# Kernel optimization log

Measured on AMD Instinct MI355X. Metric: run time of the kernel, lower is better.

The kernel has to match this reference:

```python
import jax, jax.numpy as jnp
import numpy as np

HID = 4096      # hidden_size
H = 32          # num_attention_heads
K = 8           # num_key_value_heads
D = HID // H    # head_dim = 128
G = H // K      # q heads per kv group = 4
INTER = 14336   # intermediate_size
T = 2048        # tokens (prefill)
EPS = 1e-5
THETA = 1000000.0


def setup_inputs() -> dict:
    key = jax.random.key(0)
    ks = jax.random.split(key, 9)
    s = 0.02
    return {
        "hidden_states": jax.random.normal(ks[0], (T, HID), jnp.float32),
        "position_ids": jnp.arange(T, dtype=jnp.int64),
        "wqkv": jax.random.normal(ks[1], ((H + 2 * K) * D, HID), jnp.float32) * s,
        "wo": jax.random.normal(ks[2], (HID, HID), jnp.float32) * s,
        "w1": jax.random.normal(ks[3], (INTER, HID), jnp.float32) * s,  # gate
        "w3": jax.random.normal(ks[4], (INTER, HID), jnp.float32) * s,  # up
        "w2": jax.random.normal(ks[5], (HID, INTER), jnp.float32) * s,  # down
        "attn_norm_w": jnp.ones((HID,), jnp.float32),
        "ffn_norm_w": jnp.ones((HID,), jnp.float32),
    }


def _rmsnorm(x, w):
    var = jnp.mean(jnp.square(x), axis=-1, keepdims=True)
    return x * jax.lax.rsqrt(var + EPS) * w


def _rope(x, cos, sin):
    # non-interleaved (half-split) rotation; x: [T, h, D], cos/sin: [T, 1, D//2]
    x1, x2 = x[..., : D // 2], x[..., D // 2 :]
    return jnp.concatenate([x1 * cos - x2 * sin, x2 * cos + x1 * sin], axis=-1)


def _attention(x, position_ids, wqkv, wo):
    t = x.shape[0]
    qkv = x @ wqkv.T  # [T, (H+2K)*D]
    q = qkv[:, : H * D].reshape(t, H, D)
    k = qkv[:, H * D : (H + K) * D].reshape(t, K, D)
    v = qkv[:, (H + K) * D :].reshape(t, K, D)

    inv_freq = 1.0 / (THETA ** (jnp.arange(0, D, 2, dtype=jnp.float32) / D))
    freqs = position_ids.astype(jnp.float32)[:, None] * inv_freq  # [T, D//2]
    cos = jnp.cos(freqs)[:, None, :]
    sin = jnp.sin(freqs)[:, None, :]
    q = _rope(q, cos, sin)
    k = _rope(k, cos, sin)

    # grouped-query attention: [T, K, G, D] queries vs [T, K, D] keys
    qg = q.reshape(t, K, G, D)
    scale = 1.0 / jnp.sqrt(jnp.float32(D))
    scores = jnp.einsum("tkgd,skd->kgts", qg, k) * scale  # [K, G, T, T]
    causal = jnp.tril(jnp.ones((t, t), dtype=bool))
    scores = jnp.where(causal, scores, jnp.finfo(scores.dtype).min)
    probs = jax.nn.softmax(scores, axis=-1)
    out = jnp.einsum("kgts,skd->tkgd", probs, v).reshape(t, H * D)
    return out @ wo.T


def _mlp(x, w1, w3, w2):
    return (jax.nn.silu(x @ w1.T) * (x @ w3.T)) @ w2.T


def reference(hidden_states, position_ids, wqkv, wo, w1, w3, w2, attn_norm_w, ffn_norm_w):
    h = hidden_states + _attention(_rmsnorm(hidden_states, attn_norm_w), position_ids, wqkv, wo)
    return h + _mlp(_rmsnorm(h, ffn_norm_w), w1, w3, w2)
```

## Files before the change

kernel.cpp:

```cpp
#include <hip/hip_runtime.h>
#include <stdint.h>

#define T_SEQ 2048
#define HIDN  4096
#define NH    32
#define NKV   8
#define DH    128
#define INTER 14336
#define QKV_N 6144
#define EPSR  1e-5f
#define SCALE 0.08838834764831845f
#define KVB   64

typedef __bf16 bf16x8 __attribute__((ext_vector_type(8)));
typedef float  f32x4  __attribute__((ext_vector_type(4)));

__device__ __forceinline__ f32x4 mfma16(bf16x8 a, bf16x8 b, f32x4 c) {
  return __builtin_amdgcn_mfma_f32_16x16x32_bf16(a, b, c, 0, 0, 0);
}

__device__ __forceinline__ void glds16(const void* g, void* l) {
  __builtin_amdgcn_global_load_lds(
      (__attribute__((address_space(1))) void*)g,
      (__attribute__((address_space(3))) void*)l,
      16, 0, 0);
}

__global__ __launch_bounds__(256) void cvt_bf16_kernel(
    const float* __restrict__ src, __bf16* __restrict__ dst, long n) {
  long stride = (long)gridDim.x * 256 * 8;
  for (long i = ((long)blockIdx.x * 256 + threadIdx.x) * 8; i < n; i += stride) {
    float4 a = *(const float4*)(src + i);
    float4 b = *(const float4*)(src + i + 4);
    bf16x8 o;
    o[0]=(__bf16)a.x; o[1]=(__bf16)a.y; o[2]=(__bf16)a.z; o[3]=(__bf16)a.w;
    o[4]=(__bf16)b.x; o[5]=(__bf16)b.y; o[6]=(__bf16)b.z; o[7]=(__bf16)b.w;
    *(bf16x8*)(dst + i) = o;
  }
}

__global__ __launch_bounds__(256) void rmsnorm_kernel(
    const float* __restrict__ x, const float* __restrict__ w,
    __bf16* __restrict__ y) {
  const int row = blockIdx.x, tid = threadIdx.x;
  const float* xr = x + (size_t)row * HIDN + tid * 16;
  float4 v0 = ((const float4*)xr)[0];
  float4 v1 = ((const float4*)xr)[1];
  float4 v2 = ((const float4*)xr)[2];
  float4 v3 = ((const float4*)xr)[3];
  float ss = v0.x*v0.x + v0.y*v0.y + v0.z*v0.z + v0.w*v0.w
           + v1.x*v1.x + v1.y*v1.y + v1.z*v1.z + v1.w*v1.w
           + v2.x*v2.x + v2.y*v2.y + v2.z*v2.z + v2.w*v2.w
           + v3.x*v3.x + v3.y*v3.y + v3.z*v3.z + v3.w*v3.w;
  #pragma unroll
  for (int off = 32; off >= 1; off >>= 1) ss += __shfl_xor(ss, off, 64);
  __shared__ float red[4];
  if ((tid & 63) == 0) red[tid >> 6] = ss;
  __syncthreads();
  float rn = rsqrtf((red[0] + red[1] + red[2] + red[3]) * (1.0f / HIDN) + EPSR);
  const float* wr = w + tid * 16;
  float4 w0 = ((const float4*)wr)[0];
  float4 w1v = ((const float4*)wr)[1];
  float4 w2v = ((const float4*)wr)[2];
  float4 w3v = ((const float4*)wr)[3];
  bf16x8 o0, o1;
  o0[0]=(__bf16)(v0.x*rn*w0.x);  o0[1]=(__bf16)(v0.y*rn*w0.y);
  o0[2]=(__bf16)(v0.z*rn*w0.z);  o0[3]=(__bf16)(v0.w*rn*w0.w);
  o0[4]=(__bf16)(v1.x*rn*w1v.x); o0[5]=(__bf16)(v1.y*rn*w1v.y);
  o0[6]=(__bf16)(v1.z*rn*w1v.z); o0[7]=(__bf16)(v1.w*rn*w1v.w);
  o1[0]=(__bf16)(v2.x*rn*w2v.x); o1[1]=(__bf16)(v2.y*rn*w2v.y);
  o1[2]=(__bf16)(v2.z*rn*w2v.z); o1[3]=(__bf16)(v2.w*rn*w2v.w);
  o1[4]=(__bf16)(v3.x*rn*w3v.x); o1[5]=(__bf16)(v3.y*rn*w3v.y);
  o1[6]=(__bf16)(v3.z*rn*w3v.z); o1[7]=(__bf16)(v3.w*rn*w3v.w);
  __bf16* yo = y + (size_t)row * HIDN + tid * 16;
  *(bf16x8*)(yo)     = o0;
  *(bf16x8*)(yo + 8) = o1;
}

template<int EPI>
__global__ __launch_bounds__(512, 2) void gemm256_kernel(
    const __bf16* __restrict__ A, const __bf16* __restrict__ B,
    void* __restrict__ Cout, int M, int N, int Kfull, int KZ) {
  extern __shared__ __align__(16) char smem[];
  const int tid = threadIdx.x;
  const int lane = tid & 63;
  const int wv = tid >> 6;
  const int wm = wv >> 2;
  const int wn = wv & 3;
  const int lr = lane & 15, q = lane >> 4;

  const int gx = gridDim.x, gy = gridDim.y;
  const int nwg = gx * gy;
  const int orig = blockIdx.y * gx + blockIdx.x;
  const int cpx = nwg >> 3;
  const int swz = (orig & 7) * cpx + (orig >> 3);
  const int by = swz % gy, bx = swz / gy;
  const int m0 = by * 256, n0 = bx * 256;
  const int kbase = blockIdx.z * KZ;
  const int NT = KZ >> 5;

  const char* aS[2]; const char* bS[2]; int Lds[2];
  #pragma unroll
  for (int j = 0; j < 2; j++) {
    int L = j * 512 + tid;
    int row = L >> 2;
    int s = (L & 3) ^ ((row >> 1) & 3);
    aS[j] = (const char*)(A + (size_t)(m0 + row) * Kfull + kbase + s * 8);
    bS[j] = (const char*)(B + (size_t)(n0 + row) * Kfull + kbase + s * 8);
    Lds[j] = L * 16;
  }

  const int sA = q ^ ((lr >> 1) & 3);
  int aoff[8], boff[4];
  #pragma unroll
  for (int mt = 0; mt < 8; mt++) aoff[mt] = (wm * 128 + mt * 16 + lr) * 64 + sA * 16;
  #pragma unroll
  for (int nt = 0; nt < 4; nt++) boff[nt] = 16384 + (wn * 64 + nt * 16 + lr) * 64 + sA * 16;

#define STAGE_T(tile, sb) do {                                   \
    char* _b = smem + (sb) * 32768;                              \
    size_t _ko = (size_t)(tile) * 64;                            \
    glds16(aS[0] + _ko, _b + Lds[0]);                            \
    glds16(aS[1] + _ko, _b + Lds[1]);                            \
    glds16(bS[0] + _ko, _b + 16384 + Lds[0]);                    \
    glds16(bS[1] + _ko, _b + 16384 + Lds[1]);                    \
  } while (0)

#define GBODY(VMC, DOST) do {                                    \
    if (DOST) { STAGE_T(t + 3, sbufi); sbufi = (sbufi == 4) ? 0 : sbufi + 1; } \
    asm volatile("s_waitcnt vmcnt(" #VMC ")" ::: "memory");      \
    __builtin_amdgcn_s_barrier();                                \
    asm volatile("" ::: "memory");                               \
    __builtin_amdgcn_sched_barrier(0);                           \
    { const char* _bA = smem + bufi * 32768;                     \
      bf16x8 bf[4], af[8];                                       \
      _Pragma("unroll") for (int nt = 0; nt < 4; nt++)           \
        bf[nt] = *(const bf16x8*)(_bA + boff[nt]);               \
      _Pragma("unroll") for (int mt = 0; mt < 8; mt++)           \
        af[mt] = *(const bf16x8*)(_bA + aoff[mt]);               \
      __builtin_amdgcn_s_setprio(1);                             \
      _Pragma("unroll") for (int mt = 0; mt < 8; mt++)           \
        _Pragma("unroll") for (int nt = 0; nt < 4; nt++)         \
          acc[mt][nt] = mfma16(af[mt], bf[nt], acc[mt][nt]);     \
      __builtin_amdgcn_s_setprio(0); }                           \
    bufi = (bufi == 4) ? 0 : bufi + 1;                           \
  } while (0)

  f32x4 acc[8][4] = {};
  STAGE_T(0, 0); STAGE_T(1, 1); STAGE_T(2, 2);
  int bufi = 0, sbufi = 3;
  for (int t = 0; t < NT - 3; ++t) GBODY(12, true);
  { int t = 0; (void)t;
    GBODY(8, false); GBODY(4, false); GBODY(0, false); }
#undef STAGE_T
#undef GBODY

  #pragma unroll
  for (int mt = 0; mt < 8; mt++) {
    #pragma unroll
    for (int r = 0; r < 4; r++) {
      int rr = m0 + wm * 128 + mt * 16 + q * 4 + r;
      #pragma unroll
      for (int nt = 0; nt < 4; nt++) {
        int cc = n0 + wn * 64 + nt * 16 + lr;
        size_t ix = (size_t)rr * N + cc;
        float val = acc[mt][nt][r];
        if (EPI == 0) ((float*)Cout)[(size_t)blockIdx.z * M * N + ix] = val;
        else          ((__bf16*)Cout)[ix] = (__bf16)val;
      }
    }
  }
}

__global__ __launch_bounds__(256) void add3_kernel(
    const float* __restrict__ p, const float* __restrict__ r,
    float* __restrict__ o, long n) {
  long stride = (long)gridDim.x * 1024;
  for (long i = ((long)blockIdx.x * 256 + threadIdx.x) * 4; i < n; i += stride) {
    float4 a = *(const float4*)(p + i);
    float4 b = *(const float4*)(p + n + i);
    float4 c = *(const float4*)(r + i);
    float4 o4;
    o4.x = a.x + b.x + c.x; o4.y = a.y + b.y + c.y;
    o4.z = a.z + b.z + c.z; o4.w = a.w + b.w + c.w;
    *(float4*)(o + i) = o4;
  }
}

__global__ __launch_bounds__(256) void rope_kernel(
    const __bf16* __restrict__ qkv, __bf16* __restrict__ q_r,
    __bf16* __restrict__ k_r) {
  const int t = blockIdx.x, tid = threadIdx.x;
  __shared__ float cs[64], sn[64];
  if (tid < 64) {
    float inv = exp2f(-(float)tid * (19.931568569324174f / 64.0f));
    float f = (float)t * inv;
    cs[tid] = cosf(f);
    sn[tid] = sinf(f);
  }
  __syncthreads();
  const __bf16* row = qkv + (size_t)t * QKV_N;
  for (int it = tid; it < 40 * 64; it += 256) {
    int hh = it >> 6, i = it & 63;
    float x1 = (float)row[hh * 128 + i];
    float x2 = (float)row[hh * 128 + 64 + i];
    float c = cs[i], s = sn[i];
    float o1 = x1 * c - x2 * s;
    float o2 = x2 * c + x1 * s;
    if (hh < NH) {
      __bf16* qo = q_r + (size_t)t * HIDN + hh * 128;
      qo[i] = (__bf16)o1;
      qo[64 + i] = (__bf16)o2;
    } else {
      __bf16* ko = k_r + (size_t)t * (NKV * DH) + (hh - NH) * 128;
      ko[i] = (__bf16)o1;
      ko[64 + i] = (__bf16)o2;
    }
  }
}

__global__ __launch_bounds__(256) void vtrans_kernel(
    const __bf16* __restrict__ qkv, __bf16* __restrict__ v_t) {
  __shared__ __bf16 tile[64][136];
  const int tid = threadIdx.x;
  const int t0 = blockIdx.x * 64, kh = blockIdx.y;
  #pragma unroll
  for (int i = 0; i < 4; i++) {
    int u = i * 256 + tid;
    int row = u >> 4, c = (u & 15) * 8;
    *(bf16x8*)&tile[row][c] =
        *(const bf16x8*)(qkv + (size_t)(t0 + row) * QKV_N + (NH + NKV) * DH + kh * DH + c);
  }
  __syncthreads();
  const int d = tid & 127, th = (tid >> 7) * 32;
  #pragma unroll
  for (int j = 0; j < 4; j++) {
    int t = th + j * 8;
    bf16x8 o;
    #pragma unroll
    for (int e = 0; e < 8; e++) o[e] = tile[t + e][d];
    *(bf16x8*)(v_t + ((size_t)kh * DH + d) * T_SEQ + t0 + t) = o;
  }
}

__global__ __launch_bounds__(256) void attn_kernel(
    const __bf16* __restrict__ q_r, const __bf16* __restrict__ k_r,
    const __bf16* __restrict__ v_t, __bf16* __restrict__ attn_o) {
  __shared__ __align__(16) __bf16 Ks[KVB * 128];
  __shared__ __align__(16) __bf16 Vs[128 * KVB];
  __shared__ __align__(16) __bf16 Pl[4 * 16 * KVB];

  const int tid = threadIdx.x;
  const int lane = tid & 63, wv = tid >> 6;
  const int lr = lane & 15, g = lane >> 4;
  const int qt = gridDim.x - 1 - blockIdx.x;
  const int h = blockIdx.y;
  const int kh = h >> 2;
  const int q0b = qt * 64;
  const int q0w = q0b + wv * 16;

  bf16x8 qf[4];
  {
    const __bf16* qp = q_r + (size_t)(q0w + lr) * HIDN + h * DH + g * 8;
    #pragma unroll
    for (int kk = 0; kk < 4; kk++) qf[kk] = *(const bf16x8*)(qp + kk * 32);
  }

  f32x4 o[8] = {};
  float mrun[4] = {-1e30f, -1e30f, -1e30f, -1e30f};
  float lrun[4] = {0.f, 0.f, 0.f, 0.f};
  char* PlW = (char*)Pl + wv * 2048;

  for (int kv0 = 0; kv0 < q0b + KVB; kv0 += KVB) {
    __syncthreads();
    #pragma unroll
    for (int i = 0; i < 4; i++) {
      int u = i * 256 + tid;
      int row = u >> 4;
      int cb = ((u & 15) * 16) ^ ((row & 7) << 4);
      glds16((const char*)(k_r + (size_t)(kv0 + row) * (NKV * DH) + kh * DH) + cb,
             (char*)Ks + u * 16);
    }
    #pragma unroll
    for (int i = 0; i < 4; i++) {
      int u = i * 256 + tid;
      int row = u >> 3;
      int cb = ((u & 7) * 16) ^ ((row & 7) << 4);
      glds16((const char*)(v_t + ((size_t)kh * DH + row) * T_SEQ + kv0) + cb,
             (char*)Vs + u * 16);
    }
    __syncthreads();

    if (q0w + 15 >= kv0) {
      f32x4 s[4] = {};
      #pragma unroll
      for (int kk = 0; kk < 4; kk++) {
        #pragma unroll
        for (int jt = 0; jt < 4; jt++) {
          int krow = jt * 16 + lr;
          int cb = (kk * 64 + g * 16) ^ ((krow & 7) << 4);
          bf16x8 kf = *(const bf16x8*)((char*)Ks + krow * 256 + cb);
          s[jt] = mfma16(qf[kk], kf, s[jt]);
        }
      }
      const bool need_mask = (kv0 + KVB - 1) > q0w;
      #pragma unroll
      for (int r = 0; r < 4; r++) {
        int qpos = q0w + g * 4 + r;
        int prow = g * 4 + r;
        float p[4];
        #pragma unroll
        for (int jt = 0; jt < 4; jt++) {
          float v = s[jt][r] * SCALE;
          if (need_mask && (kv0 + jt * 16 + lr > qpos)) v = -1e30f;
          p[jt] = v;
        }
        float mx = fmaxf(fmaxf(p[0], p[1]), fmaxf(p[2], p[3]));
        #pragma unroll
        for (int off = 1; off < 16; off <<= 1) mx = fmaxf(mx, __shfl_xor(mx, off, 64));
        float mn = fmaxf(mrun[r], mx);
        float corr = __expf(mrun[r] - mn);
        mrun[r] = mn;
        float ps = 0.f;
        #pragma unroll
        for (int jt = 0; jt < 4; jt++) {
          p[jt] = __expf(p[jt] - mn);
          ps += p[jt];
          int cbyte = ((jt * 16 + lr) * 2) ^ ((prow & 7) << 4);
          *(__bf16*)(PlW + prow * 128 + cbyte) = (__bf16)p[jt];
        }
        #pragma unroll
        for (int off = 1; off < 16; off <<= 1) ps += __shfl_xor(ps, off, 64);
        lrun[r] = lrun[r] * corr + ps;
        #pragma unroll
        for (int nt = 0; nt < 8; nt++) o[nt][r] *= corr;
      }
      bf16x8 pa[2];
      #pragma unroll
      for (int ks = 0; ks < 2; ks++)
        pa[ks] = *(const bf16x8*)(PlW + lr * 128 + ((g * 16 + ks * 64) ^ ((lr & 7) << 4)));
      #pragma unroll
      for (int nt = 0; nt < 8; nt++) {
        #pragma unroll
        for (int ks = 0; ks < 2; ks++) {
          int vrow = nt * 16 + lr;
          int cb = (ks * 64 + g * 16) ^ ((vrow & 7) << 4);
          bf16x8 vf = *(const bf16x8*)((char*)Vs + vrow * 128 + cb);
          o[nt] = mfma16(pa[ks], vf, o[nt]);
        }
      }
    }
  }

  #pragma unroll
  for (int nt = 0; nt < 8; nt++) {
    #pragma unroll
    for (int r = 0; r < 4; r++) {
      int qrow = q0w + g * 4 + r;
      int d = nt * 16 + lr;
      attn_o[(size_t)qrow * HIDN + h * DH + d] = (__bf16)(o[nt][r] / lrun[r]);
    }
  }
}

__global__ __launch_bounds__(256) void silu_mul_kernel(
    const __bf16* __restrict__ u, const __bf16* __restrict__ v,
    __bf16* __restrict__ g, long n) {
  long stride = (long)gridDim.x * 256 * 8;
  for (long i = ((long)blockIdx.x * 256 + threadIdx.x) * 8; i < n; i += stride) {
    bf16x8 uu = *(const bf16x8*)(u + i);
    bf16x8 vv = *(const bf16x8*)(v + i);
    bf16x8 gg;
    #pragma unroll
    for (int j = 0; j < 8; j++) {
      float x = (float)uu[j];
      float y = (float)vv[j];
      float sl = x / (1.0f + __expf(-x));
      gg[j] = (__bf16)(sl * y);
    }
    *(bf16x8*)(g + i) = gg;
  }
}

extern "C" void kernel_launch(void* const* d_in, const int* in_sizes, int n_in,
                              void* d_out, int out_size, void* d_ws, size_t ws_size,
                              hipStream_t stream) {
  const float* hidden = (const float*)d_in[0];
  const float* wqkv = (const float*)d_in[2];
  const float* wo   = (const float*)d_in[3];
  const float* w1   = (const float*)d_in[4];
  const float* w3   = (const float*)d_in[5];
  const float* w2   = (const float*)d_in[6];
  const float* anw  = (const float*)d_in[7];
  const float* fnw  = (const float*)d_in[8];

  char* ws = (char*)d_ws;
  const size_t SZ_XN   = (size_t)T_SEQ * HIDN * 2;
  const size_t SZ_QKV  = (size_t)T_SEQ * QKV_N * 2;
  const size_t SZ_KR   = (size_t)T_SEQ * NKV * DH * 2;
  const size_t SZ_H    = (size_t)T_SEQ * HIDN * 4;
  const size_t SZ_UV   = (size_t)T_SEQ * INTER * 2;

  const size_t W_QKV = (size_t)QKV_N * HIDN * 2;
  const size_t W_O   = (size_t)HIDN * HIDN * 2;
  const size_t W_I   = (size_t)INTER * HIDN * 2;
  const size_t W_TOTAL = W_QKV + W_O + 3 * W_I;

  char* act = ws + W_TOTAL;

  __bf16* xn1    = (__bf16*)(act);
  __bf16* qkv    = (__bf16*)(act + SZ_XN);
  __bf16* q_r    = (__bf16*)(act + SZ_XN + SZ_QKV);
  __bf16* ubuf   = (__bf16*)(act);
  __bf16* k_r    = (__bf16*)(act + SZ_UV);
  __bf16* attn_o = (__bf16*)(act + SZ_UV + SZ_KR);
  float*  hbuf   = (float*) (act + SZ_UV + SZ_KR + SZ_XN);
  __bf16* v_t    = (__bf16*)(act + SZ_UV + SZ_KR + SZ_XN);
  __bf16* xn2    = (__bf16*)(act + SZ_UV + SZ_KR + SZ_XN + SZ_H);
  __bf16* vbuf   = (__bf16*)(act + SZ_UV + SZ_KR + SZ_XN + SZ_H + SZ_XN);
  __bf16* gbuf   = ubuf;
  float*  pbuf   = (float*)(act + SZ_UV + SZ_KR + SZ_XN + SZ_H);

  __bf16* wqkv_b = (__bf16*)(ws);
  __bf16* wo_b   = (__bf16*)(ws + W_QKV);
  __bf16* w1_b   = (__bf16*)(ws + W_QKV + W_O);
  __bf16* w3_b   = (__bf16*)(ws + W_QKV + W_O + W_I);
  __bf16* w2_b   = (__bf16*)(ws + W_QKV + W_O + 2 * W_I);

  const int LDS_BYTES = 163840;
  hipFuncSetAttribute((const void*)gemm256_kernel<0>,
                      hipFuncAttributeMaxDynamicSharedMemorySize, LDS_BYTES);
  hipFuncSetAttribute((const void*)gemm256_kernel<1>,
                      hipFuncAttributeMaxDynamicSharedMemorySize, LDS_BYTES);

  cvt_bf16_kernel<<<2048, 256, 0, stream>>>(wqkv, wqkv_b, (long)QKV_N * HIDN);
  cvt_bf16_kernel<<<2048, 256, 0, stream>>>(wo,   wo_b,   (long)HIDN * HIDN);
  cvt_bf16_kernel<<<2048, 256, 0, stream>>>(w1,   w1_b,   (long)INTER * HIDN);
  cvt_bf16_kernel<<<2048, 256, 0, stream>>>(w3,   w3_b,   (long)INTER * HIDN);
  cvt_bf16_kernel<<<2048, 256, 0, stream>>>(w2,   w2_b,   (long)HIDN * INTER);

  rmsnorm_kernel<<<T_SEQ, 256, 0, stream>>>(hidden, anw, xn1);
  gemm256_kernel<1><<<dim3(QKV_N / 256, T_SEQ / 256, 1), 512, LDS_BYTES, stream>>>(
      xn1, wqkv_b, qkv, T_SEQ, QKV_N, HIDN, HIDN);
  rope_kernel<<<T_SEQ, 256, 0, stream>>>(qkv, q_r, k_r);
  vtrans_kernel<<<dim3(T_SEQ / 64, NKV), 256, 0, stream>>>(qkv, v_t);
  attn_kernel<<<dim3(T_SEQ / 64, NH), 256, 0, stream>>>(q_r, k_r, v_t, attn_o);
  gemm256_kernel<0><<<dim3(HIDN / 256, T_SEQ / 256, 2), 512, LDS_BYTES, stream>>>(
      attn_o, wo_b, pbuf, T_SEQ, HIDN, HIDN, HIDN / 2);
  add3_kernel<<<2048, 256, 0, stream>>>(pbuf, hidden, hbuf, (long)T_SEQ * HIDN);
  rmsnorm_kernel<<<T_SEQ, 256, 0, stream>>>(hbuf, fnw, xn2);
  gemm256_kernel<1><<<dim3(INTER / 256, T_SEQ / 256, 1), 512, LDS_BYTES, stream>>>(
      xn2, w1_b, ubuf, T_SEQ, INTER, HIDN, HIDN);
  gemm256_kernel<1><<<dim3(INTER / 256, T_SEQ / 256, 1), 512, LDS_BYTES, stream>>>(
      xn2, w3_b, vbuf, T_SEQ, INTER, HIDN, HIDN);
  silu_mul_kernel<<<2048, 256, 0, stream>>>(ubuf, vbuf, gbuf, (long)T_SEQ * INTER);
  gemm256_kernel<0><<<dim3(HIDN / 256, T_SEQ / 256, 2), 512, LDS_BYTES, stream>>>(
      gbuf, w2_b, pbuf, T_SEQ, HIDN, INTER, INTER / 2);
  add3_kernel<<<2048, 256, 0, stream>>>(pbuf, hbuf, (float*)d_out, (long)T_SEQ * HIDN);
}
```

Baseline: 1.342 ms.

## Switch to 128x256 GEMM tiles, fuse gate/up with SiLU, fuse add+rmsnorm

Replaces the 256x256, 512-thread GEMM with a 128x256, 256-thread tile that uses a 3-stage buffer ring and register fragment preloading. The w1 and w3 weights are interleaved during bf16 conversion so one GEMM computes both gate and up, with SiLU-multiply applied in its epilogue. The separate silu kernel and the u/v intermediate buffers go away. The residual add is also fused with the second RMSNorm. Smaller tiles raise the block count but lower per-block data reuse and change the pipelining depth.

Result: no change. 1.367 ms (+1.9%).

```diff
diff --git a/kernel.cpp b/kernel.cpp
--- a/kernel.cpp
+++ b/kernel.cpp
@@ -36,6 +36,30 @@
     o[0]=(__bf16)a.x; o[1]=(__bf16)a.y; o[2]=(__bf16)a.z; o[3]=(__bf16)a.w;
     o[4]=(__bf16)b.x; o[5]=(__bf16)b.y; o[6]=(__bf16)b.z; o[7]=(__bf16)b.w;
     *(bf16x8*)(dst + i) = o;
+  }
+}
+
+__global__ __launch_bounds__(256) void cvt_w13_kernel(
+    const float* __restrict__ w1, const float* __restrict__ w3,
+    __bf16* __restrict__ dst) {
+  for (int c = blockIdx.x; c < 2 * INTER; c += gridDim.x) {
+    int tau = c >> 8, j2 = c & 255;
+    int wn = j2 >> 7, j = j2 & 127, nt = j >> 4, k16 = j & 15;
+    const float* src = (nt < 4 ? w1 : w3) +
+        (size_t)(tau * 128 + wn * 64 + (nt & 3) * 16 + k16) * HIDN;
+    __bf16* d = dst + (size_t)c * HIDN;
+    int i = threadIdx.x * 16;
+    float4 a = *(const float4*)(src + i);
+    float4 b = *(const float4*)(src + i + 4);
+    float4 e = *(const float4*)(src + i + 8);
+    float4 f = *(const float4*)(src + i + 12);
+    bf16x8 o0, o1;
+    o0[0]=(__bf16)a.x; o0[1]=(__bf16)a.y; o0[2]=(__bf16)a.z; o0[3]=(__bf16)a.w;
+    o0[4]=(__bf16)b.x; o0[5]=(__bf16)b.y; o0[6]=(__bf16)b.z; o0[7]=(__bf16)b.w;
+    o1[0]=(__bf16)e.x; o1[1]=(__bf16)e.y; o1[2]=(__bf16)e.z; o1[3]=(__bf16)e.w;
+    o1[4]=(__bf16)f.x; o1[5]=(__bf16)f.y; o1[6]=(__bf16)f.z; o1[7]=(__bf16)f.w;
+    *(bf16x8*)(d + i) = o0;
+    *(bf16x8*)(d + i + 8) = o1;
   }
 }
 
@@ -59,35 +83,67 @@
   __syncthreads();
   float rn = rsqrtf((red[0] + red[1] + red[2] + red[3]) * (1.0f / HIDN) + EPSR);
   const float* wr = w + tid * 16;
-  float4 w0 = ((const float4*)wr)[0];
-  float4 w1v = ((const float4*)wr)[1];
-  float4 w2v = ((const float4*)wr)[2];
-  float4 w3v = ((const float4*)wr)[3];
-  bf16x8 o0, o1;
-  o0[0]=(__bf16)(v0.x*rn*w0.x);  o0[1]=(__bf16)(v0.y*rn*w0.y);
-  o0[2]=(__bf16)(v0.z*rn*w0.z);  o0[3]=(__bf16)(v0.w*rn*w0.w);
-  o0[4]=(__bf16)(v1.x*rn*w1v.x); o0[5]=(__bf16)(v1.y*rn*w1v.y);
-  o0[6]=(__bf16)(v1.z*rn*w1v.z); o0[7]=(__bf16)(v1.w*rn*w1v.w);
-  o1[0]=(__bf16)(v2.x*rn*w2v.x); o1[1]=(__bf16)(v2.y*rn*w2v.y);
-  o1[2]=(__bf16)(v2.z*rn*w2v.z); o1[3]=(__bf16)(v2.w*rn*w2v.w);
-  o1[4]=(__bf16)(v3.x*rn*w3v.x); o1[5]=(__bf16)(v3.y*rn*w3v.y);
-  o1[6]=(__bf16)(v3.z*rn*w3v.z); o1[7]=(__bf16)(v3.w*rn*w3v.w);
-  __bf16* yo = y + (size_t)row * HIDN + tid * 16;
-  *(bf16x8*)(yo)     = o0;
-  *(bf16x8*)(yo + 8) = o1;
+  #pragma unroll
+  for (int h = 0; h < 2; h++) {
+    float4 a = ((const float4*)xr)[h*2], b = ((const float4*)xr)[h*2+1];
+    float4 wa = ((const float4*)wr)[h*2], wb = ((const float4*)wr)[h*2+1];
+    bf16x8 o;
+    o[0]=(__bf16)(a.x*rn*wa.x); o[1]=(__bf16)(a.y*rn*wa.y);
+    o[2]=(__bf16)(a.z*rn*wa.z); o[3]=(__bf16)(a.w*rn*wa.w);
+    o[4]=(__bf16)(b.x*rn*wb.x); o[5]=(__bf16)(b.y*rn*wb.y);
+    o[6]=(__bf16)(b.z*rn*wb.z); o[7]=(__bf16)(b.w*rn*wb.w);
+    *(bf16x8*)(y + (size_t)row * HIDN + tid * 16 + h * 8) = o;
+  }
+}
+
+__global__ __launch_bounds__(256) void add3_rms_kernel(
+    const float* __restrict__ p, const float* __restrict__ resid,
+    const float* __restrict__ w, float* __restrict__ hout,
+    __bf16* __restrict__ xn) {
+  const int row = blockIdx.x, tid = threadIdx.x;
+  const size_t base = (size_t)row * HIDN + tid * 16;
+  const size_t half = (size_t)T_SEQ * HIDN;
+  float h[16];
+  float ss = 0.f;
+  #pragma unroll
+  for (int q = 0; q < 4; q++) {
+    float4 a = *(const float4*)(p + base + q * 4);
+    float4 b = *(const float4*)(p + half + base + q * 4);
+    float4 c = *(const float4*)(resid + base + q * 4);
+    h[q*4+0] = a.x + b.x + c.x; h[q*4+1] = a.y + b.y + c.y;
+    h[q*4+2] = a.z + b.z + c.z; h[q*4+3] = a.w + b.w + c.w;
+    ss += h[q*4]*h[q*4] + h[q*4+1]*h[q*4+1] + h[q*4+2]*h[q*4+2] + h[q*4+3]*h[q*4+3];
+    *(float4*)(hout + base + q * 4) = *(float4*)&h[q*4];
+  }
+  #pragma unroll
+  for (int off = 32; off >= 1; off >>= 1) ss += __shfl_xor(ss, off, 64);
+  __shared__ float red[4];
+  if ((tid & 63) == 0) red[tid >> 6] = ss;
+  __syncthreads();
+  float rn = rsqrtf((red[0] + red[1] + red[2] + red[3]) * (1.0f / HIDN) + EPSR);
+  #pragma unroll
+  for (int hb = 0; hb < 2; hb++) {
+    bf16x8 o;
+    #pragma unroll
+    for (int e = 0; e < 8; e++) {
+      float wv = w[tid * 16 + hb * 8 + e];
+      o[e] = (__bf16)(h[hb*8+e] * rn * wv);
+    }
+    *(bf16x8*)(xn + base + hb * 8) = o;
+  }
 }
 
 template<int EPI>
-__global__ __launch_bounds__(512, 2) void gemm256_kernel(
+__global__ __launch_bounds__(256, 2) void gemm128_kernel(
     const __bf16* __restrict__ A, const __bf16* __restrict__ B,
-    void* __restrict__ Cout, int M, int N, int Kfull, int KZ) {
+    void* __restrict__ Cout, int M, int N, int Kfull, int KZ, int Nout) {
   extern __shared__ __align__(16) char smem[];
   const int tid = threadIdx.x;
   const int lane = tid & 63;
   const int wv = tid >> 6;
-  const int wm = wv >> 2;
-  const int wn = wv & 3;
-  const int lr = lane & 15, q = lane >> 4;
+  const int wm = wv >> 1;
+  const int wn = wv & 1;
+  const int lr = lane & 15, ql = lane >> 4;
 
   const int gx = gridDim.x, gy = gridDim.y;
   const int nwg = gx * gy;
@@ -95,78 +151,112 @@
   const int cpx = nwg >> 3;
   const int swz = (orig & 7) * cpx + (orig >> 3);
   const int by = swz % gy, bx = swz / gy;
-  const int m0 = by * 256, n0 = bx * 256;
+  const int m0 = by * 128, n0 = bx * 256;
   const int kbase = blockIdx.z * KZ;
   const int NT = KZ >> 5;
 
-  const char* aS[2]; const char* bS[2]; int Lds[2];
-  #pragma unroll
-  for (int j = 0; j < 2; j++) {
-    int L = j * 512 + tid;
-    int row = L >> 2;
-    int s = (L & 3) ^ ((row >> 1) & 3);
-    aS[j] = (const char*)(A + (size_t)(m0 + row) * Kfull + kbase + s * 8);
-    bS[j] = (const char*)(B + (size_t)(n0 + row) * Kfull + kbase + s * 8);
-    Lds[j] = L * 16;
-  }
-
-  const int sA = q ^ ((lr >> 1) & 3);
-  int aoff[8], boff[4];
-  #pragma unroll
-  for (int mt = 0; mt < 8; mt++) aoff[mt] = (wm * 128 + mt * 16 + lr) * 64 + sA * 16;
-  #pragma unroll
-  for (int nt = 0; nt < 4; nt++) boff[nt] = 16384 + (wn * 64 + nt * 16 + lr) * 64 + sA * 16;
-
-#define STAGE_T(tile, sb) do {                                   \
-    char* _b = smem + (sb) * 32768;                              \
-    size_t _ko = (size_t)(tile) * 64;                            \
-    glds16(aS[0] + _ko, _b + Lds[0]);                            \
-    glds16(aS[1] + _ko, _b + Lds[1]);                            \
-    glds16(bS[0] + _ko, _b + 16384 + Lds[0]);                    \
-    glds16(bS[1] + _ko, _b + 16384 + Lds[1]);                    \
+  const char* gS[6]; int lD[6];
+  #pragma unroll
+  for (int j = 0; j < 6; j++) {
+    int u = (j < 2) ? (j * 256 + tid) : (512 + (j - 2) * 256 + tid);
+    if (j < 2) {
+      int row = u >> 2;
+      int s = (u & 3) ^ ((row >> 1) & 3);
+      gS[j] = (const char*)(A + (size_t)(m0 + row) * Kfull + kbase) + s * 16;
+      lD[j] = u * 16;
+    } else {
+      int u2 = u - 512;
+      int row = u2 >> 2;
+      int s = (u2 & 3) ^ ((row >> 1) & 3);
+      gS[j] = (const char*)(B + (size_t)(n0 + row) * Kfull + kbase) + s * 16;
+      lD[j] = 8192 + u2 * 16;
+    }
+  }
+
+  const int sA = ql ^ ((lr >> 1) & 3);
+  int aoff[4], boff[8];
+  #pragma unroll
+  for (int mt = 0; mt < 4; mt++) aoff[mt] = (wm * 64 + mt * 16 + lr) * 64 + sA * 16;
+  #pragma unroll
+  for (int nt = 0; nt < 8; nt++) boff[nt] = 8192 + (wn * 128 + nt * 16 + lr) * 64 + sA * 16;
+
+#define STAGE(t, b) do {                                           \
+    const size_t _o = (size_t)(t) * 64;                            \
+    char* _d = smem + (b) * 24576;                                 \
+    glds16(gS[0] + _o, _d + lD[0]); glds16(gS[1] + _o, _d + lD[1]);\
+    glds16(gS[2] + _o, _d + lD[2]); glds16(gS[3] + _o, _d + lD[3]);\
+    glds16(gS[4] + _o, _d + lD[4]); glds16(gS[5] + _o, _d + lD[5]);\
   } while (0)
-
-#define GBODY(VMC, DOST) do {                                    \
-    if (DOST) { STAGE_T(t + 3, sbufi); sbufi = (sbufi == 4) ? 0 : sbufi + 1; } \
-    asm volatile("s_waitcnt vmcnt(" #VMC ")" ::: "memory");      \
-    __builtin_amdgcn_s_barrier();                                \
-    asm volatile("" ::: "memory");                               \
-    __builtin_amdgcn_sched_barrier(0);                           \
-    { const char* _bA = smem + bufi * 32768;                     \
-      bf16x8 bf[4], af[8];                                       \
-      _Pragma("unroll") for (int nt = 0; nt < 4; nt++)           \
-        bf[nt] = *(const bf16x8*)(_bA + boff[nt]);               \
-      _Pragma("unroll") for (int mt = 0; mt < 8; mt++)           \
-        af[mt] = *(const bf16x8*)(_bA + aoff[mt]);               \
-      __builtin_amdgcn_s_setprio(1);                             \
-      _Pragma("unroll") for (int mt = 0; mt < 8; mt++)           \
-        _Pragma("unroll") for (int nt = 0; nt < 4; nt++)         \
-          acc[mt][nt] = mfma16(af[mt], bf[nt], acc[mt][nt]);     \
-      __builtin_amdgcn_s_setprio(0); }                           \
-    bufi = (bufi == 4) ? 0 : bufi + 1;                           \
+#define LOADFRAGS(b) do {                                          \
+    const char* _p = smem + (b) * 24576;                           \
+    _Pragma("unroll") for (int _m = 0; _m < 4; _m++)               \
+      af[_m] = *(const bf16x8*)(_p + aoff[_m]);                    \
+    _Pragma("unroll") for (int _n = 0; _n < 8; _n++)               \
+      bf[_n] = *(const bf16x8*)(_p + boff[_n]);                    \
   } while (0)
-
-  f32x4 acc[8][4] = {};
-  STAGE_T(0, 0); STAGE_T(1, 1); STAGE_T(2, 2);
-  int bufi = 0, sbufi = 3;
-  for (int t = 0; t < NT - 3; ++t) GBODY(12, true);
-  { int t = 0; (void)t;
-    GBODY(8, false); GBODY(4, false); GBODY(0, false); }
-#undef STAGE_T
-#undef GBODY
-
-  #pragma unroll
-  for (int mt = 0; mt < 8; mt++) {
+#define WAITK() do { asm volatile("s_waitcnt lgkmcnt(0)" ::: "memory"); \
+    __builtin_amdgcn_sched_barrier(0); } while (0)
+#define MFMA32() do {                                              \
+    __builtin_amdgcn_s_setprio(1);                                 \
+    _Pragma("unroll") for (int _m = 0; _m < 4; _m++)               \
+      _Pragma("unroll") for (int _n = 0; _n < 8; _n++)             \
+        acc[_m][_n] = mfma16(af[_m], bf[_n], acc[_m][_n]);         \
+    __builtin_amdgcn_s_setprio(0);                                 \
+  } while (0)
+#define INC3(v) v = (v == 2) ? 0 : v + 1
+
+  f32x4 acc[4][8] = {};
+  bf16x8 af[4], bf[8];
+
+  STAGE(0, 0); STAGE(1, 1);
+  int bufi = 0, sbufi = 2;
+  for (int t = 0; t < NT - 2; ++t) {
+    asm volatile("s_waitcnt vmcnt(6)" ::: "memory");
+    __builtin_amdgcn_s_barrier();
+    LOADFRAGS(bufi);
+    STAGE(t + 2, sbufi);
+    WAITK(); MFMA32();
+    INC3(bufi); INC3(sbufi);
+  }
+  asm volatile("s_waitcnt vmcnt(6)" ::: "memory");
+  __builtin_amdgcn_s_barrier();
+  LOADFRAGS(bufi);
+  WAITK(); MFMA32();
+  INC3(bufi);
+  asm volatile("s_waitcnt vmcnt(0)" ::: "memory");
+  __builtin_amdgcn_s_barrier();
+  LOADFRAGS(bufi);
+  WAITK(); MFMA32();
+
+#undef STAGE
+#undef LOADFRAGS
+#undef WAITK
+#undef MFMA32
+#undef INC3
+
+  #pragma unroll
+  for (int mt = 0; mt < 4; mt++) {
     #pragma unroll
     for (int r = 0; r < 4; r++) {
-      int rr = m0 + wm * 128 + mt * 16 + q * 4 + r;
-      #pragma unroll
-      for (int nt = 0; nt < 4; nt++) {
-        int cc = n0 + wn * 64 + nt * 16 + lr;
-        size_t ix = (size_t)rr * N + cc;
-        float val = acc[mt][nt][r];
-        if (EPI == 0) ((float*)Cout)[(size_t)blockIdx.z * M * N + ix] = val;
-        else          ((__bf16*)Cout)[ix] = (__bf16)val;
+      int rr = m0 + wm * 64 + mt * 16 + ql * 4 + r;
+      if (EPI == 2) {
+        #pragma unroll
+        for (int nt = 0; nt < 4; nt++) {
+          float u = acc[mt][nt][r];
+          float v = acc[mt][nt + 4][r];
+          float g = u / (1.0f + __expf(-u)) * v;
+          int cc = (n0 >> 1) + wn * 64 + nt * 16 + lr;
+          ((__bf16*)Cout)[(size_t)rr * Nout + cc] = (__bf16)g;
+        }
+      } else {
+        #pragma unroll
+        for (int nt = 0; nt < 8; nt++) {
+          int cc = n0 + wn * 128 + nt * 16 + lr;
+          size_t ix = (size_t)rr * N + cc;
+          float val = acc[mt][nt][r];
+          if (EPI == 0) ((float*)Cout)[(size_t)blockIdx.z * M * N + ix] = val;
+          else          ((__bf16*)Cout)[ix] = (__bf16)val;
+        }
       }
     }
   }
@@ -363,25 +453,6 @@
   }
 }
 
-__global__ __launch_bounds__(256) void silu_mul_kernel(
-    const __bf16* __restrict__ u, const __bf16* __restrict__ v,
-    __bf16* __restrict__ g, long n) {
-  long stride = (long)gridDim.x * 256 * 8;
-  for (long i = ((long)blockIdx.x * 256 + threadIdx.x) * 8; i < n; i += stride) {
-    bf16x8 uu = *(const bf16x8*)(u + i);
-    bf16x8 vv = *(const bf16x8*)(v + i);
-    bf16x8 gg;
-    #pragma unroll
-    for (int j = 0; j < 8; j++) {
-      float x = (float)uu[j];
-      float y = (float)vv[j];
-      float sl = x / (1.0f + __expf(-x));
-      gg[j] = (__bf16)(sl * y);
-    }
-    *(bf16x8*)(g + i) = gg;
-  }
-}
-
 extern "C" void kernel_launch(void* const* d_in, const int* in_sizes, int n_in,
                               void* d_out, int out_size, void* d_ws, size_t ws_size,
                               hipStream_t stream) {
@@ -411,50 +482,44 @@
   __bf16* xn1    = (__bf16*)(act);
   __bf16* qkv    = (__bf16*)(act + SZ_XN);
   __bf16* q_r    = (__bf16*)(act + SZ_XN + SZ_QKV);
-  __bf16* ubuf   = (__bf16*)(act);
+  __bf16* gbuf   = (__bf16*)(act);
   __bf16* k_r    = (__bf16*)(act + SZ_UV);
   __bf16* attn_o = (__bf16*)(act + SZ_UV + SZ_KR);
   float*  hbuf   = (float*) (act + SZ_UV + SZ_KR + SZ_XN);
   __bf16* v_t    = (__bf16*)(act + SZ_UV + SZ_KR + SZ_XN);
   __bf16* xn2    = (__bf16*)(act + SZ_UV + SZ_KR + SZ_XN + SZ_H);
-  __bf16* vbuf   = (__bf16*)(act + SZ_UV + SZ_KR + SZ_XN + SZ_H + SZ_XN);
-  __bf16* gbuf   = ubuf;
-  float*  pbuf   = (float*)(act + SZ_UV + SZ_KR + SZ_XN + SZ_H);
+  float*  pbuf   = (float*)(act + SZ_UV + SZ_KR + SZ_XN + SZ_H + SZ_XN);
 
   __bf16* wqkv_b = (__bf16*)(ws);
   __bf16* wo_b   = (__bf16*)(ws + W_QKV);
-  __bf16* w1_b   = (__bf16*)(ws + W_QKV + W_O);
-  __bf16* w3_b   = (__bf16*)(ws + W_QKV + W_O + W_I);
+  __bf16* w13_b  = (__bf16*)(ws + W_QKV + W_O);
   __bf16* w2_b   = (__bf16*)(ws + W_QKV + W_O + 2 * W_I);
 
-  const int LDS_BYTES = 163840;
-  hipFuncSetAttribute((const void*)gemm256_kernel<0>,
+  const int LDS_BYTES = 73728;
+  hipFuncSetAttribute((const void*)gemm128_kernel<0>,
                       hipFuncAttributeMaxDynamicSharedMemorySize, LDS_BYTES);
-  hipFuncSetAttribute((const void*)gemm256_kernel<1>,
+  hipFuncSetAttribute((const void*)gemm128_kernel<1>,
+                      hipFuncAttributeMaxDynamicSharedMemorySize, LDS_BYTES);
+  hipFuncSetAttribute((const void*)gemm128_kernel<2>,
                       hipFuncAttributeMaxDynamicSharedMemorySize, LDS_BYTES);
 
   cvt_bf16_kernel<<<2048, 256, 0, stream>>>(wqkv, wqkv_b, (long)QKV_N * HIDN);
   cvt_bf16_kernel<<<2048, 256, 0, stream>>>(wo,   wo_b,   (long)HIDN * HIDN);
-  cvt_bf16_kernel<<<2048, 256, 0, stream>>>(w1,   w1_b,   (long)INTER * HIDN);
-  cvt_bf16_kernel<<<2048, 256, 0, stream>>>(w3,   w3_b,   (long)INTER * HIDN);
+  cvt_w13_kernel<<<2048, 256, 0, stream>>>(w1, w3, w13_b);
   cvt_bf16_kernel<<<2048, 256, 0, stream>>>(w2,   w2_b,   (long)HIDN * INTER);
 
   rmsnorm_kernel<<<T_SEQ, 256, 0, stream>>>(hidden, anw, xn1);
-  gemm256_kernel<1><<<dim3(QKV_N / 256, T_SEQ / 256, 1), 512, LDS_BYTES, stream>>>(
-      xn1, wqkv_b, qkv, T_SEQ, QKV_N, HIDN, HIDN);
+  gemm128_kernel<1><<<dim3(QKV_N / 256, T_SEQ / 128, 1), 256, LDS_BYTES, stream>>>(
+      xn1, wqkv_b, qkv, T_SEQ, QKV_N, HIDN, HIDN, QKV_N);
   rope_kernel<<<T_SEQ, 256, 0, stream>>>(qkv, q_r, k_r);
   vtrans_kernel<<<dim3(T_SEQ / 64, NKV), 256, 0, stream>>>(qkv, v_t);
   attn_kernel<<<dim3(T_SEQ / 64, NH), 256, 0, stream>>>(q_r, k_r, v_t, attn_o);
-  gemm256_kernel<0><<<dim3(HIDN / 256, T_SEQ / 256, 2), 512, LDS_BYTES, stream>>>(
-      attn_o, wo_b, pbuf, T_SEQ, HIDN, HIDN, HIDN / 2);
-  add3_kernel<<<2048, 256, 0, stream>>>(pbuf, hidden, hbuf, (long)T_SEQ * HIDN);
-  rmsnorm_kernel<<<T_SEQ, 256, 0, stream>>>(hbuf, fnw, xn2);
-  gemm256_kernel<1><<<dim3(INTER / 256, T_SEQ / 256, 1), 512, LDS_BYTES, stream>>>(
-      xn2, w1_b, ubuf, T_SEQ, INTER, HIDN, HIDN);
-  gemm256_kernel<1><<<dim3(INTER / 256, T_SEQ / 256, 1), 512, LDS_BYTES, stream>>>(
-      xn2, w3_b, vbuf, T_SEQ, INTER, HIDN, HIDN);
-  silu_mul_kernel<<<2048, 256, 0, stream>>>(ubuf, vbuf, gbuf, (long)T_SEQ * INTER);
-  gemm256_kernel<0><<<dim3(HIDN / 256, T_SEQ / 256, 2), 512, LDS_BYTES, stream>>>(
-      gbuf, w2_b, pbuf, T_SEQ, HIDN, INTER, INTER / 2);
+  gemm128_kernel<0><<<dim3(HIDN / 256, T_SEQ / 128, 2), 256, LDS_BYTES, stream>>>(
+      attn_o, wo_b, pbuf, T_SEQ, HIDN, HIDN, HIDN / 2, HIDN);
+  add3_rms_kernel<<<T_SEQ, 256, 0, stream>>>(pbuf, hidden, fnw, hbuf, xn2);
+  gemm128_kernel<2><<<dim3(2 * INTER / 256, T_SEQ / 128, 1), 256, LDS_BYTES, stream>>>(
+      xn2, w13_b, gbuf, T_SEQ, 2 * INTER, HIDN, HIDN, INTER);
+  gemm128_kernel<0><<<dim3(HIDN / 256, T_SEQ / 128, 2), 256, LDS_BYTES, stream>>>(
+      gbuf, w2_b, pbuf, T_SEQ, HIDN, INTER, INTER / 2, HIDN);
   add3_kernel<<<2048, 256, 0, stream>>>(pbuf, hbuf, (float*)d_out, (long)T_SEQ * HIDN);
 }
```
